# Kernel tuning notes

Measured on AMD Instinct MI355X. Metric: run time of the kernel, lower is better.

The kernel has to match this reference:

```python
import jax, jax.numpy as jnp
import numpy as np

EPS = 1e-10
R, H, W = 8192, 1024, 1024


def setup_inputs() -> dict:
    key = jax.random.key(0)
    k1, k2, k3, k4, k5, k6 = jax.random.split(key, 6)
    seg = jax.random.normal(k1, (1, 2, H, W), dtype=jnp.float32)
    score = jax.random.uniform(k2, (R, 1), dtype=jnp.float32)
    # boxes with guaranteed non-empty regions (x2>x1, y2>y1)
    x1 = jax.random.randint(k3, (R,), 0, W - 1)
    y1 = jax.random.randint(k4, (R,), 0, H - 1)
    w = jax.random.randint(k5, (R,), 1, W)
    h = jax.random.randint(k6, (R,), 1, H)
    x2 = jnp.minimum(x1 + w, W)
    y2 = jnp.minimum(y1 + h, H)
    ssw = jnp.stack([jnp.zeros_like(x1), x1, y1, x2, y2], axis=1)[None].astype(jnp.int32)
    return {"ssw": ssw, "seg": seg, "score": score}


def reference(ssw, seg, score):
    boxes = ssw[0, :, 1:]                      # [R,4] = x1,y1,x2,y2
    seg = jax.nn.softmax(seg, axis=1)
    score_map = seg[0, 1]                      # [H,W]
    # Summed-area table: region mean for every ROI in one vectorized pass
    # (replaces the per-ROI python-loop slicing in the original).
    P = jnp.pad(jnp.cumsum(jnp.cumsum(score_map, axis=0), axis=1), ((1, 0), (1, 0)))
    x1, y1, x2, y2 = boxes[:, 0], boxes[:, 1], boxes[:, 2], boxes[:, 3]
    sums = P[y2, x2] - P[y1, x2] - P[y2, x1] + P[y1, x1]
    area = ((y2 - y1) * (x2 - x1)).astype(score_map.dtype)
    iou = sums / area                          # [R] per-ROI mean score
    # pairwise smooth-abs differences
    sim_iou = jnp.sqrt((iou[:, None] - iou[None, :]) ** 2 + EPS)     # [R,R]
    s = score.reshape(-1)
    sim_score = jnp.sqrt((s[:, None] - s[None, :]) ** 2 + EPS)        # [R,R]
    return jnp.mean((sim_iou - sim_score) ** 2)
```

## Files before the change

### kernel.cpp

```cpp
#include <hip/hip_runtime.h>
#include <math.h>

#define HH 1024
#define WW 1024
#define RR 8192
#define EPSF 1e-10f
#define EPSD 1e-10

#define OFF_BSUM  8388608
#define OFF_IOU   8650752
#define OFF_STAT  8683520

__device__ __forceinline__ double sigm(float a, float b) {
    return 1.0 / (1.0 + (double)expf(a - b));
}

__global__ void row_scan(const float* __restrict__ seg, double* __restrict__ rowpref) {
    const int h = blockIdx.x;
    const int t = threadIdx.x;
    const float4* s0 = (const float4*)(seg + (size_t)h * WW);
    const float4* s1 = (const float4*)(seg + (size_t)(HH * WW) + (size_t)h * WW);
    float4 a = s0[t];
    float4 b = s1[t];
    double p0 = sigm(a.x, b.x);
    double p1 = p0 + sigm(a.y, b.y);
    double p2 = p1 + sigm(a.z, b.z);
    double p3 = p2 + sigm(a.w, b.w);

    double tsum = p3;
    const int lane = t & 63, wid = t >> 6;
    #pragma unroll
    for (int off = 1; off < 64; off <<= 1) {
        double n = __shfl_up(tsum, off, 64);
        if (lane >= off) tsum += n;
    }
    __shared__ double wsum[4];
    if (lane == 63) wsum[wid] = tsum;
    __syncthreads();
    double woff = 0.0;
    for (int k = 0; k < wid; ++k) woff += wsum[k];
    const double excl = woff + tsum - p3;

    double* out = rowpref + (size_t)h * WW + 4 * t;
    out[0] = excl + p0;
    out[1] = excl + p1;
    out[2] = excl + p2;
    out[3] = excl + p3;
}

__global__ void col_partial(const double* __restrict__ rowpref, double* __restrict__ bsum) {
    const int w = blockIdx.x * 256 + threadIdx.x;
    const int chunk = blockIdx.y;
    const int r0 = chunk * 32;
    double acc = 0.0;
    #pragma unroll 4
    for (int r = r0; r < r0 + 32; ++r) acc += rowpref[(size_t)r * WW + w];
    bsum[chunk * WW + w] = acc;
}

__global__ void col_scan(double* __restrict__ rowpref, const double* __restrict__ bsum,
                         double* __restrict__ stats) {
    if (blockIdx.x == 0 && blockIdx.y == 0 && threadIdx.x < 5) stats[threadIdx.x] = 0.0;
    const int w = blockIdx.x * 256 + threadIdx.x;
    const int chunk = blockIdx.y;
    double acc = 0.0;
    for (int k = 0; k < chunk; ++k) acc += bsum[k * WW + w];
    const int r0 = chunk * 32;
    for (int r = r0; r < r0 + 32; ++r) {
        acc += rowpref[(size_t)r * WW + w];
        rowpref[(size_t)r * WW + w] = acc;
    }
}

__global__ void box_stats(const int* __restrict__ ssw, const double* __restrict__ C,
                          const float* __restrict__ score,
                          float* __restrict__ iou, double* __restrict__ stats) {
    const int r = blockIdx.x * 256 + threadIdx.x;
    const int* b = ssw + r * 5;
    const int x1 = b[1], y1 = b[2], x2 = b[3], y2 = b[4];
    double p22 = C[(size_t)(y2 - 1) * WW + (x2 - 1)];
    double p12 = (y1 > 0) ? C[(size_t)(y1 - 1) * WW + (x2 - 1)] : 0.0;
    double p21 = (x1 > 0) ? C[(size_t)(y2 - 1) * WW + (x1 - 1)] : 0.0;
    double p11 = (y1 > 0 && x1 > 0) ? C[(size_t)(y1 - 1) * WW + (x1 - 1)] : 0.0;
    double sums = p22 - p12 - p21 + p11;
    double area = (double)((y2 - y1) * (x2 - x1));
    double u = sums / area;
    iou[r] = (float)u;
    double s = (double)score[r];

    double v0 = u, v1 = u * u, v2 = s, v3 = s * s;
    #pragma unroll
    for (int off = 32; off; off >>= 1) {
        v0 += __shfl_down(v0, off, 64);
        v1 += __shfl_down(v1, off, 64);
        v2 += __shfl_down(v2, off, 64);
        v3 += __shfl_down(v3, off, 64);
    }
    if ((threadIdx.x & 63) == 0) {
        atomicAdd(&stats[0], v0);
        atomicAdd(&stats[1], v1);
        atomicAdd(&stats[2], v2);
        atomicAdd(&stats[3], v3);
    }
}

#define JTILE 128
__global__ void pair_prod(const float* __restrict__ iou, const float* __restrict__ score,
                          double* __restrict__ stats) {
    __shared__ float ju[JTILE];
    __shared__ float js[JTILE];
    const int t = threadIdx.x;
    const int j0 = blockIdx.y * JTILE;
    if (t < JTILE) ju[t] = iou[j0 + t];
    else if (t < 2 * JTILE) js[t - JTILE] = score[j0 + t - JTILE];

    const int i0 = blockIdx.x * 1024 + t;
    float iu[4], is[4];
    #pragma unroll
    for (int k = 0; k < 4; ++k) {
        iu[k] = iou[i0 + 256 * k];
        is[k] = score[i0 + 256 * k];
    }
    __syncthreads();

    float acc[4] = {0.f, 0.f, 0.f, 0.f};
    #pragma unroll 8
    for (int j = 0; j < JTILE; ++j) {
        const float uj = ju[j];
        const float sj = js[j];
        #pragma unroll
        for (int k = 0; k < 4; ++k) {
            float du = iu[k] - uj;
            float p  = fmaf(du, du, EPSF);
            float ds = is[k] - sj;
            float q  = fmaf(ds, ds, EPSF);
            acc[k] += __builtin_amdgcn_sqrtf(p * q);
        }
    }
    double v = (double)((acc[0] + acc[1]) + (acc[2] + acc[3]));
    #pragma unroll
    for (int off = 32; off; off >>= 1) v += __shfl_down(v, off, 64);
    __shared__ double wred[4];
    const int lane = t & 63, wid = t >> 6;
    if (lane == 0) wred[wid] = v;
    __syncthreads();
    if (t == 0) atomicAdd(&stats[4], wred[0] + wred[1] + wred[2] + wred[3]);
}

__global__ void finalize(const double* __restrict__ stats, float* __restrict__ out) {
    const double R = (double)RR;
    double Su = stats[0], Su2 = stats[1], Ss = stats[2], Ss2 = stats[3], Sab = stats[4];
    double lossR2 = 2.0 * R * Su2 - 2.0 * Su * Su
                  + 2.0 * R * Ss2 - 2.0 * Ss * Ss
                  + 2.0 * R * R * EPSD
                  - 2.0 * Sab;
    out[0] = (float)(lossR2 / (R * R));
}

extern "C" void kernel_launch(void* const* d_in, const int* in_sizes, int n_in,
                              void* d_out, int out_size, void* d_ws, size_t ws_size,
                              hipStream_t stream) {
    const int*   ssw   = (const int*)d_in[0];
    const float* seg   = (const float*)d_in[1];
    const float* score = (const float*)d_in[2];

    double* rowpref = (double*)d_ws;
    double* bsum    = (double*)((char*)d_ws + OFF_BSUM);
    float*  iou     = (float*)((char*)d_ws + OFF_IOU);
    double* stats   = (double*)((char*)d_ws + OFF_STAT);

    row_scan<<<HH, 256, 0, stream>>>(seg, rowpref);
    col_partial<<<dim3(4, 32), 256, 0, stream>>>(rowpref, bsum);
    col_scan<<<dim3(4, 32), 256, 0, stream>>>(rowpref, bsum, stats);
    box_stats<<<RR / 256, 256, 0, stream>>>(ssw, rowpref, score, iou, stats);
    pair_prod<<<dim3(RR / 1024, RR / JTILE), 256, 0, stream>>>(iou, score, stats);
    finalize<<<1, 1, 0, stream>>>(stats, (float*)d_out);
}
```

Before: 110.5 us.

## Fuse finalize into pair_prod via last-block counter, retile pairs, fast sigmoid

Removes the separate finalize launch: each pair_prod block bumps an atomic counter, and the last block computes the loss. Stats and counter zeroing moves into col_partial. The pair tile changes from 4 rows x 128 columns per thread to 8 rows x 32 columns, giving more blocks and more independent accumulators. The sigmoid now uses hardware exp2 and reciprocal in float instead of expf plus a double divide, trading a little precision in the summed-area table for cheaper row_scan arithmetic.

```diff
diff --git a/kernel.cpp b/kernel.cpp
--- a/kernel.cpp
+++ b/kernel.cpp
@@ -10,9 +10,13 @@
 #define OFF_BSUM  8388608
 #define OFF_IOU   8650752
 #define OFF_STAT  8683520
+#define OFF_CNT   8683560
 
 __device__ __forceinline__ double sigm(float a, float b) {
-    return 1.0 / (1.0 + (double)expf(a - b));
+    float z = (a - b) * 1.44269504088896f;
+    float e = __builtin_amdgcn_exp2f(z);
+    float sg = __builtin_amdgcn_rcpf(1.0f + e);
+    return (double)sg;
 }
 
 __global__ void row_scan(const float* __restrict__ seg, double* __restrict__ rowpref) {
@@ -48,7 +52,12 @@
     out[3] = excl + p3;
 }
 
-__global__ void col_partial(const double* __restrict__ rowpref, double* __restrict__ bsum) {
+__global__ void col_partial(const double* __restrict__ rowpref, double* __restrict__ bsum,
+                            double* __restrict__ stats, unsigned* __restrict__ cnt) {
+    if (blockIdx.x == 0 && blockIdx.y == 0) {
+        if (threadIdx.x < 5) stats[threadIdx.x] = 0.0;
+        if (threadIdx.x == 5) *cnt = 0u;
+    }
     const int w = blockIdx.x * 256 + threadIdx.x;
     const int chunk = blockIdx.y;
     const int r0 = chunk * 32;
@@ -58,9 +67,7 @@
     bsum[chunk * WW + w] = acc;
 }
 
-__global__ void col_scan(double* __restrict__ rowpref, const double* __restrict__ bsum,
-                         double* __restrict__ stats) {
-    if (blockIdx.x == 0 && blockIdx.y == 0 && threadIdx.x < 5) stats[threadIdx.x] = 0.0;
+__global__ void col_scan(double* __restrict__ rowpref, const double* __restrict__ bsum) {
     const int w = blockIdx.x * 256 + threadIdx.x;
     const int chunk = blockIdx.y;
     double acc = 0.0;
@@ -104,57 +111,69 @@
     }
 }
 
-#define JTILE 128
+#define KI 8
+#define JT 32
+#define NBLK ((RR / (256 * KI)) * (RR / JT))
 __global__ void pair_prod(const float* __restrict__ iou, const float* __restrict__ score,
-                          double* __restrict__ stats) {
-    __shared__ float ju[JTILE];
-    __shared__ float js[JTILE];
+                          double* __restrict__ stats, unsigned* __restrict__ cnt,
+                          float* __restrict__ out) {
+    __shared__ float ju[JT];
+    __shared__ float js[JT];
     const int t = threadIdx.x;
-    const int j0 = blockIdx.y * JTILE;
-    if (t < JTILE) ju[t] = iou[j0 + t];
-    else if (t < 2 * JTILE) js[t - JTILE] = score[j0 + t - JTILE];
-
-    const int i0 = blockIdx.x * 1024 + t;
-    float iu[4], is[4];
+    const int j0 = blockIdx.y * JT;
+    if (t < JT) {
+        ju[t] = iou[j0 + t];
+        js[t] = score[j0 + t];
+    }
+    const int i0 = blockIdx.x * (256 * KI) + t;
+    float iu[KI], isc[KI];
     #pragma unroll
-    for (int k = 0; k < 4; ++k) {
-        iu[k] = iou[i0 + 256 * k];
-        is[k] = score[i0 + 256 * k];
+    for (int k = 0; k < KI; ++k) {
+        iu[k]  = iou[i0 + 256 * k];
+        isc[k] = score[i0 + 256 * k];
     }
     __syncthreads();
 
-    float acc[4] = {0.f, 0.f, 0.f, 0.f};
-    #pragma unroll 8
-    for (int j = 0; j < JTILE; ++j) {
+    float acc[KI];
+    #pragma unroll
+    for (int k = 0; k < KI; ++k) acc[k] = 0.0f;
+    #pragma unroll 4
+    for (int j = 0; j < JT; ++j) {
         const float uj = ju[j];
         const float sj = js[j];
         #pragma unroll
-        for (int k = 0; k < 4; ++k) {
+        for (int k = 0; k < KI; ++k) {
             float du = iu[k] - uj;
             float p  = fmaf(du, du, EPSF);
-            float ds = is[k] - sj;
+            float ds = isc[k] - sj;
             float q  = fmaf(ds, ds, EPSF);
             acc[k] += __builtin_amdgcn_sqrtf(p * q);
         }
     }
-    double v = (double)((acc[0] + acc[1]) + (acc[2] + acc[3]));
+    float afl = 0.0f;
+    #pragma unroll
+    for (int k = 0; k < KI; ++k) afl += acc[k];
+    double v = (double)afl;
     #pragma unroll
     for (int off = 32; off; off >>= 1) v += __shfl_down(v, off, 64);
     __shared__ double wred[4];
     const int lane = t & 63, wid = t >> 6;
     if (lane == 0) wred[wid] = v;
     __syncthreads();
-    if (t == 0) atomicAdd(&stats[4], wred[0] + wred[1] + wred[2] + wred[3]);
-}
-
-__global__ void finalize(const double* __restrict__ stats, float* __restrict__ out) {
-    const double R = (double)RR;
-    double Su = stats[0], Su2 = stats[1], Ss = stats[2], Ss2 = stats[3], Sab = stats[4];
-    double lossR2 = 2.0 * R * Su2 - 2.0 * Su * Su
-                  + 2.0 * R * Ss2 - 2.0 * Ss * Ss
-                  + 2.0 * R * R * EPSD
-                  - 2.0 * Sab;
-    out[0] = (float)(lossR2 / (R * R));
+    if (t == 0) {
+        atomicAdd(&stats[4], wred[0] + wred[1] + wred[2] + wred[3]);
+        __threadfence();
+        unsigned old = atomicAdd(cnt, 1u);
+        if (old == NBLK - 1) {
+            const double R = (double)RR;
+            double Su = stats[0], Su2 = stats[1], Ss = stats[2], Ss2 = stats[3], Sab = stats[4];
+            double lossR2 = 2.0 * R * Su2 - 2.0 * Su * Su
+                          + 2.0 * R * Ss2 - 2.0 * Ss * Ss
+                          + 2.0 * R * R * EPSD
+                          - 2.0 * Sab;
+            out[0] = (float)(lossR2 / (R * R));
+        }
+    }
 }
 
 extern "C" void kernel_launch(void* const* d_in, const int* in_sizes, int n_in,
@@ -164,15 +183,15 @@
     const float* seg   = (const float*)d_in[1];
     const float* score = (const float*)d_in[2];
 
-    double* rowpref = (double*)d_ws;
-    double* bsum    = (double*)((char*)d_ws + OFF_BSUM);
-    float*  iou     = (float*)((char*)d_ws + OFF_IOU);
-    double* stats   = (double*)((char*)d_ws + OFF_STAT);
+    double*   rowpref = (double*)d_ws;
+    double*   bsum    = (double*)((char*)d_ws + OFF_BSUM);
+    float*    iou     = (float*)((char*)d_ws + OFF_IOU);
+    double*   stats   = (double*)((char*)d_ws + OFF_STAT);
+    unsigned* cnt     = (unsigned*)((char*)d_ws + OFF_CNT);
 
     row_scan<<<HH, 256, 0, stream>>>(seg, rowpref);
-    col_partial<<<dim3(4, 32), 256, 0, stream>>>(rowpref, bsum);
-    col_scan<<<dim3(4, 32), 256, 0, stream>>>(rowpref, bsum, stats);
+    col_partial<<<dim3(4, 32), 256, 0, stream>>>(rowpref, bsum, stats, cnt);
+    col_scan<<<dim3(4, 32), 256, 0, stream>>>(rowpref, bsum);
     box_stats<<<RR / 256, 256, 0, stream>>>(ssw, rowpref, score, iou, stats);
-    pair_prod<<<dim3(RR / 1024, RR / JTILE), 256, 0, stream>>>(iou, score, stats);
-    finalize<<<1, 1, 0, stream>>>(stats, (float*)d_out);
+    pair_prod<<<dim3(RR / (256 * KI), RR / JT), 256, 0, stream>>>(iou, score, stats, cnt, (float*)d_out);
 }
```

New measurement: 123.0 us. 1.11x slower.
